# Kernel optimization log

Hardware: AMD Instinct MI355X
Metric: run time of the kernel (lower is better)

Reference implementation:

```python
import jax, jax.numpy as jnp
import numpy as np

E = 1024          # n_embed_dim
H = 64            # head_size = n_embed_dim // n_heads (16)

def setup_inputs() -> dict:
    key = jax.random.key(0)
    k_x, k_q, k_k, k_v = jax.random.split(key, 4)
    scale = 1.0 / np.sqrt(E)
    return {
        "x": jax.random.normal(k_x, (4, 2048, E), dtype=jnp.float32),
        "ln_gamma": jnp.ones((E,), jnp.float32),
        "ln_beta": jnp.zeros((E,), jnp.float32),
        # torch nn.Linear weights: [out_features, in_features]
        "Wq": jax.random.normal(k_q, (H, E), dtype=jnp.float32) * scale,
        "Wk": jax.random.normal(k_k, (H, E), dtype=jnp.float32) * scale,
        "Wv": jax.random.normal(k_v, (H, E), dtype=jnp.float32) * scale,
    }

def reference(x, ln_gamma, ln_beta, Wq, Wk, Wv):
    # LayerNorm over last dim (eps matches torch default 1e-5)
    mu = jnp.mean(x, axis=-1, keepdims=True)
    var = jnp.mean(jnp.square(x - mu), axis=-1, keepdims=True)
    xn = (x - mu) * jax.lax.rsqrt(var + 1e-5) * ln_gamma + ln_beta

    q = jnp.einsum('bse,he->bsh', xn, Wq)   # [B,S,H]
    k = jnp.einsum('bse,he->bsh', xn, Wk)
    v = jnp.einsum('bse,he->bsh', xn, Wv)

    scores = jnp.einsum('bqh,bkh->bqk', q, k) / jnp.sqrt(jnp.float32(H))
    S = x.shape[1]
    causal = jnp.tril(jnp.ones((S, S), dtype=bool))
    scores = jnp.where(causal, scores, -jnp.inf)
    attn = jax.nn.softmax(scores, axis=-1)
    return jnp.einsum('bqk,bkh->bqh', attn, v)
```

## Files before the change

### kernel.cpp

```cpp
#include <hip/hip_runtime.h>

#define E 1024
#define HH 64
#define BB 4
#define SS 2048
#define BS (BB*SS)
#define NSLOT 144

typedef unsigned short u16;
typedef short bf16x8 __attribute__((ext_vector_type(8)));
typedef float f32x4 __attribute__((ext_vector_type(4)));

#define LOG2E_O8 0.18033688011112042f

__device__ inline u16 f2bf(float f) {
    unsigned int u = __float_as_uint(f);
    unsigned int r = (u + 0x7FFFu + ((u >> 16) & 1u)) >> 16;
    return (u16)r;
}
__device__ inline float bf2f(u16 h) {
    return __uint_as_float(((unsigned int)h) << 16);
}

__global__ __launch_bounds__(256) void ln_wcast(const float* __restrict__ x,
        const float* __restrict__ gamma, const float* __restrict__ beta,
        const float* __restrict__ Wq, const float* __restrict__ Wk,
        const float* __restrict__ Wv,
        u16* __restrict__ xn, u16* __restrict__ wc) {
    const int t = threadIdx.x;
    if (blockIdx.x < 2048) {
        const int w = t >> 6, lane = t & 63;
        const size_t row = (size_t)blockIdx.x * 4 + w;
        const float4* xr = (const float4*)(x + row * E);
        float4 v[4];
        #pragma unroll
        for (int i = 0; i < 4; ++i) v[i] = xr[lane + 64 * i];
        float s = 0.f, sq = 0.f;
        #pragma unroll
        for (int i = 0; i < 4; ++i) {
            s  += v[i].x + v[i].y + v[i].z + v[i].w;
            sq += v[i].x*v[i].x + v[i].y*v[i].y + v[i].z*v[i].z + v[i].w*v[i].w;
        }
        #pragma unroll
        for (int off = 32; off > 0; off >>= 1) {
            s  += __shfl_xor(s,  off);
            sq += __shfl_xor(sq, off);
        }
        const float mean = s * (1.0f / E);
        const float var  = sq * (1.0f / E) - mean * mean;
        const float rstd = rsqrtf(var + 1e-5f);
        const float4* gr = (const float4*)gamma;
        const float4* br = (const float4*)beta;
        #pragma unroll
        for (int i = 0; i < 4; ++i) {
            const float4 g  = gr[lane + 64 * i];
            const float4 bt = br[lane + 64 * i];
            ushort4 o;
            o.x = f2bf((v[i].x - mean) * rstd * g.x + bt.x);
            o.y = f2bf((v[i].y - mean) * rstd * g.y + bt.y);
            o.z = f2bf((v[i].z - mean) * rstd * g.z + bt.z);
            o.w = f2bf((v[i].w - mean) * rstd * g.w + bt.w);
            *(ushort4*)(xn + row * E + (lane + 64 * i) * 4) = o;
        }
    } else {
        const int row = blockIdx.x - 2048;
        const float* src = (row < 64)  ? (Wq + (size_t)row * E)
                         : (row < 128) ? (Wk + (size_t)(row - 64) * E)
                                       : (Wv + (size_t)(row - 128) * E);
        const float sc = (row < 64) ? LOG2E_O8 : 1.0f;
        const float4 v = *(const float4*)(src + t * 4);
        ushort4 o;
        o.x = f2bf(v.x * sc); o.y = f2bf(v.y * sc);
        o.z = f2bf(v.z * sc); o.w = f2bf(v.w * sc);
        *(ushort4*)(wc + (size_t)row * E + t * 4) = o;
    }
}

__global__ __launch_bounds__(256) void qkv_mfma(const u16* __restrict__ xn,
        const u16* __restrict__ wc,
        u16* __restrict__ qb, u16* __restrict__ kb, u16* __restrict__ vt) {
    const int mb   = blockIdx.x >> 1;
    const int half = blockIdx.x & 1;
    const int row0 = mb * 32;
    const int t = threadIdx.x;
    const int w = t >> 6, lane = t & 63;
    const int quad = lane >> 4, r15 = lane & 15;
    const int mt = w >> 1, cgrp = w & 1;
    __shared__ u16 Xs[32 * 128];
    __shared__ u16 Ws[96 * 128];
    f32x4 acc[3] = {};
    const int xrow = mt * 16 + r15;

    for (int kc8 = 0; kc8 < 8; ++kc8) {
        __syncthreads();
        {
            const int row = t >> 3, ch = t & 7;
            #pragma unroll
            for (int hf = 0; hf < 2; ++hf) {
                const uint4 d = *(const uint4*)(xn + (size_t)(row0 + row) * E
                                                + kc8 * 128 + hf * 64 + ch * 8);
                *(uint4*)&Xs[row * 128 + hf * 64 + (ch ^ (row & 7)) * 8] = d;
            }
        }
        #pragma unroll
        for (int i = 0; i < 6; ++i) {
            const int idx = i * 256 + t;
            const int wl = idx >> 4, ch16 = idx & 15;
            const int hf = ch16 >> 3, ch = ch16 & 7;
            const uint4 d = *(const uint4*)(wc + (size_t)(half * 96 + wl) * E
                                            + kc8 * 128 + hf * 64 + ch * 8);
            *(uint4*)&Ws[wl * 128 + hf * 64 + (ch ^ (wl & 7)) * 8] = d;
        }
        __syncthreads();
        #pragma unroll
        for (int kk = 0; kk < 4; ++kk) {
            const int hf = kk >> 1, q4 = (kk & 1) * 4 + quad;
            const bf16x8 af = *(const bf16x8*)&Xs[xrow * 128 + hf * 64 + (q4 ^ (xrow & 7)) * 8];
            #pragma unroll
            for (int j = 0; j < 3; ++j) {
                const int wl = (cgrp * 3 + j) * 16 + r15;
                const bf16x8 bfr = *(const bf16x8*)&Ws[wl * 128 + hf * 64 + (q4 ^ (wl & 7)) * 8];
                acc[j] = __builtin_amdgcn_mfma_f32_16x16x32_bf16(af, bfr, acc[j], 0, 0, 0);
            }
        }
    }
    const int b    = row0 >> 11;
    const int key0 = row0 & 2047;
    #pragma unroll
    for (int j = 0; j < 3; ++j) {
        const int cg  = half * 96 + cgrp * 48 + j * 16 + r15;
        const int sel = cg >> 6;
        const int col = cg & 63;
        if (sel < 2) {
            u16* base = (sel == 0) ? qb : kb;
            #pragma unroll
            for (int r = 0; r < 4; ++r) {
                const size_t row = (size_t)row0 + mt * 16 + quad * 4 + r;
                base[row * HH + col] = f2bf(acc[j][r]);
            }
        } else {
            ushort4 pk;
            pk.x = f2bf(acc[j][0]); pk.y = f2bf(acc[j][1]);
            pk.z = f2bf(acc[j][2]); pk.w = f2bf(acc[j][3]);
            *(ushort4*)(vt + (size_t)b * HH * SS + (size_t)col * SS
                           + key0 + mt * 16 + quad * 4) = pk;
        }
    }
}

__global__ __launch_bounds__(256) void attn_partial(const u16* __restrict__ qb,
        const u16* __restrict__ kb, const u16* __restrict__ vt,
        u16* __restrict__ po, float* __restrict__ pl,
        float* __restrict__ out) {
    const int bid = blockIdx.x;
    const int b   = bid / NSLOT;
    const int s   = bid - b * NSLOT;
    int a = (int)((sqrtf(2.0f * s + 1.0f) - 1.0f) * 0.5f);
    while (2 * (a + 1) * (a + 2) <= s) ++a;
    while (2 * a * (a + 1) > s) --a;
    const int rem = s - 2 * a * (a + 1);
    const int r_  = rem / (a + 1);
    const int c   = rem - r_ * (a + 1);
    const int qt  = 4 * a + r_;
    const int nc   = a + 1;
    const int slot = b * NSLOT + s;
    const int q0   = qt << 6;
    const int t = threadIdx.x;
    const int w = t >> 6, lane = t & 63;
    const int quad = lane >> 4, r15 = lane & 15;

    __shared__ u16 Ks[4 * 64 * 64];
    __shared__ u16 VT[4 * 64 * 64];
    __shared__ u16 Ps[64 * 64];

    const size_t qrow = ((size_t)b * SS + q0 + w * 16 + r15) * HH;
    const bf16x8 qf0 = *(const bf16x8*)(qb + qrow + quad * 8);
    const bf16x8 qf1 = *(const bf16x8*)(qb + qrow + 32 + quad * 8);

    const int ntiles = min(c * 4 + 4, qt + 1) - c * 4;

    {
        const int row = t >> 2, ch0 = (t & 3) * 2;
        for (int tl = 0; tl < ntiles; ++tl) {
            const int kt = (c * 4 + tl) << 6;
            const uint4* srcK = (const uint4*)(kb + ((size_t)b * SS + kt + row) * HH + ch0 * 8);
            const uint4 k0 = srcK[0], k1 = srcK[1];
            *(uint4*)&Ks[tl * 4096 + row * 64 + ((ch0    ) ^ (row & 7)) * 8] = k0;
            *(uint4*)&Ks[tl * 4096 + row * 64 + ((ch0 + 1) ^ (row & 7)) * 8] = k1;
            const uint4* srcV = (const uint4*)(vt + (size_t)b * HH * SS + (size_t)row * SS
                                               + kt + ch0 * 8);
            const uint4 v0 = srcV[0], v1 = srcV[1];
            *(uint4*)&VT[tl * 4096 + row * 64 + ((ch0    ) ^ (row & 7)) * 8] = v0;
            *(uint4*)&VT[tl * 4096 + row * 64 + ((ch0 + 1) ^ (row & 7)) * 8] = v1;
        }
    }
    __syncthreads();

    f32x4 o[4] = {};
    float l_[4] = {0.f, 0.f, 0.f, 0.f};

    for (int tl = 0; tl < ntiles; ++tl) {
        const int tile = c * 4 + tl;
        const u16* KsT = &Ks[tl * 4096];
        const u16* VTT = &VT[tl * 4096];

        f32x4 s4[4] = {};
        #pragma unroll
        for (int nt = 0; nt < 4; ++nt) {
            const int krow = nt * 16 + r15;
            const bf16x8 k0 = *(const bf16x8*)&KsT[krow * 64 + ((    quad) ^ (krow & 7)) * 8];
            const bf16x8 k1 = *(const bf16x8*)&KsT[krow * 64 + ((4 + quad) ^ (krow & 7)) * 8];
            s4[nt] = __builtin_amdgcn_mfma_f32_16x16x32_bf16(qf0, k0, s4[nt], 0, 0, 0);
            s4[nt] = __builtin_amdgcn_mfma_f32_16x16x32_bf16(qf1, k1, s4[nt], 0, 0, 0);
        }
        if (tile == qt) {
            #pragma unroll
            for (int nt = 0; nt < 4; ++nt)
                #pragma unroll
                for (int r = 0; r < 4; ++r)
                    if (nt * 16 + r15 > w * 16 + quad * 4 + r) s4[nt][r] = -INFINITY;
        }

        float p[4][4];
        #pragma unroll
        for (int r = 0; r < 4; ++r) {
            #pragma unroll
            for (int nt = 0; nt < 4; ++nt)
                p[nt][r] = __builtin_amdgcn_exp2f(s4[nt][r]);
            l_[r] += (p[0][r] + p[1][r]) + (p[2][r] + p[3][r]);
        }

        #pragma unroll
        for (int nt = 0; nt < 4; ++nt)
            #pragma unroll
            for (int r = 0; r < 4; ++r) {
                const int prow = w * 16 + quad * 4 + r;
                const int col  = nt * 16 + r15;
                Ps[prow * 64 + (((col >> 3) ^ (prow & 7)) * 8) + (col & 7)] = f2bf(p[nt][r]);
            }
        const int arow = w * 16 + r15;
        const bf16x8 pf0 = *(const bf16x8*)&Ps[arow * 64 + ((    quad) ^ (arow & 7)) * 8];
        const bf16x8 pf1 = *(const bf16x8*)&Ps[arow * 64 + ((4 + quad) ^ (arow & 7)) * 8];

        #pragma unroll
        for (int ht = 0; ht < 4; ++ht) {
            const int vrow = ht * 16 + r15;
            const bf16x8 v0 = *(const bf16x8*)&VTT[vrow * 64 + ((    quad) ^ (vrow & 7)) * 8];
            const bf16x8 v1 = *(const bf16x8*)&VTT[vrow * 64 + ((4 + quad) ^ (vrow & 7)) * 8];
            o[ht] = __builtin_amdgcn_mfma_f32_16x16x32_bf16(pf0, v0, o[ht], 0, 0, 0);
            o[ht] = __builtin_amdgcn_mfma_f32_16x16x32_bf16(pf1, v1, o[ht], 0, 0, 0);
        }
    }

    #pragma unroll
    for (int r = 0; r < 4; ++r) {
        l_[r] += __shfl_xor(l_[r], 1); l_[r] += __shfl_xor(l_[r], 2);
        l_[r] += __shfl_xor(l_[r], 4); l_[r] += __shfl_xor(l_[r], 8);
    }

    if (nc == 1) {
        #pragma unroll
        for (int r = 0; r < 4; ++r) {
            const float inv = 1.0f / l_[r];
            const size_t orow = ((size_t)b * SS + q0 + w * 16 + quad * 4 + r) * HH;
            #pragma unroll
            for (int ht = 0; ht < 4; ++ht)
                out[orow + ht * 16 + r15] = o[ht][r] * inv;
        }
        return;
    }
    #pragma unroll
    for (int r = 0; r < 4; ++r) {
        const int q = w * 16 + quad * 4 + r;
        #pragma unroll
        for (int ht = 0; ht < 4; ++ht)
            po[(size_t)slot * 4096 + q * 64 + ht * 16 + r15] = f2bf(o[ht][r]);
        if (r15 == 0) pl[slot * 64 + q] = l_[r];
    }
}

__global__ __launch_bounds__(256) void attn_reduce(const u16* __restrict__ po,
        const float* __restrict__ pl, float* __restrict__ out) {
    const int bid = blockIdx.x;
    const int b = bid / 112, rem = bid - b * 112;
    const int qt = 4 + (rem >> 2), qq = rem & 3;
    const int a = qt >> 2, r_ = qt & 3;
    const int nc = a + 1;
    const int sbase = b * NSLOT + 2 * a * (a + 1) + r_ * (a + 1);
    const int t = threadIdx.x;
    const int h = t & 63, qr = t >> 6;
    #pragma unroll
    for (int i = 0; i < 4; ++i) {
        const int q = qq * 16 + qr * 4 + i;
        float osum = 0.f, lsum = 0.f;
        for (int cidx = 0; cidx < nc; ++cidx) {
            osum += bf2f(po[(size_t)(sbase + cidx) * 4096 + q * 64 + h]);
            lsum += pl[(sbase + cidx) * 64 + q];
        }
        out[((size_t)b * SS + (qt << 6) + q) * HH + h] = osum / lsum;
    }
}

extern "C" void kernel_launch(void* const* d_in, const int* in_sizes, int n_in,
                              void* d_out, int out_size, void* d_ws, size_t ws_size,
                              hipStream_t stream) {
    const float* x     = (const float*)d_in[0];
    const float* gamma = (const float*)d_in[1];
    const float* beta  = (const float*)d_in[2];
    const float* Wq    = (const float*)d_in[3];
    const float* Wk    = (const float*)d_in[4];
    const float* Wv    = (const float*)d_in[5];
    float* out = (float*)d_out;

    char* p = (char*)d_ws;
    u16*   xn   = (u16*)p;                         p += (size_t)BS * E * 2;
    u16*   wc   = (u16*)p;                         p += 393216;
    u16*   qb   = (u16*)p;                         p += (size_t)BS * HH * 2;
    u16*   kb   = (u16*)p;                         p += (size_t)BS * HH * 2;
    u16*   vt   = (u16*)p;                         p += (size_t)BS * HH * 2;
    u16*   po   = (u16*)p;                         p += (size_t)BB * NSLOT * 4096 * 2;
    float* pl   = (float*)p;

    ln_wcast    <<<2048 + 192,  256, 0, stream>>>(x, gamma, beta, Wq, Wk, Wv, xn, wc);
    qkv_mfma    <<<BS / 16,     256, 0, stream>>>(xn, wc, qb, kb, vt);
    attn_partial<<<BB * NSLOT,  256, 0, stream>>>(qb, kb, vt, po, pl, out);
    attn_reduce <<<BB * 112,    256, 0, stream>>>(po, pl, out);
}
```

Before: 118.8 us.

## Process two query tiles per attention block to reuse staged K/V tiles

Each attention_partial block now handles two adjacent query tiles against the same key chunk, so each K/V tile staged in LDS is used twice and the grid is halved. K and V fragments are hoisted out of the query loop into registers. In exchange, per-thread register use and work per block roughly double, and there are fewer blocks to spread across the CUs. Tiles above the diagonal are skipped for the lower query tile.

```diff
diff --git a/kernel.cpp b/kernel.cpp
--- a/kernel.cpp
+++ b/kernel.cpp
@@ -153,18 +153,16 @@
         u16* __restrict__ po, float* __restrict__ pl,
         float* __restrict__ out) {
     const int bid = blockIdx.x;
-    const int b   = bid / NSLOT;
-    const int s   = bid - b * NSLOT;
-    int a = (int)((sqrtf(2.0f * s + 1.0f) - 1.0f) * 0.5f);
-    while (2 * (a + 1) * (a + 2) <= s) ++a;
-    while (2 * a * (a + 1) > s) --a;
-    const int rem = s - 2 * a * (a + 1);
-    const int r_  = rem / (a + 1);
-    const int c   = rem - r_ * (a + 1);
-    const int qt  = 4 * a + r_;
-    const int nc   = a + 1;
-    const int slot = b * NSLOT + s;
-    const int q0   = qt << 6;
+    const int b   = bid / 72;
+    const int s2  = bid - b * 72;
+    int a = (int)((sqrtf(4.0f * s2 + 1.0f) - 1.0f) * 0.5f);
+    while ((a + 1) * (a + 2) <= s2) ++a;
+    while (a * (a + 1) > s2) --a;
+    const int rem = s2 - a * (a + 1);
+    const int rp  = rem / (a + 1);
+    const int c   = rem - rp * (a + 1);
+    const int qt0 = 4 * a + 2 * rp;
+    const int nc  = a + 1;
     const int t = threadIdx.x;
     const int w = t >> 6, lane = t & 63;
     const int quad = lane >> 4, r15 = lane & 15;
@@ -173,15 +171,19 @@
     __shared__ u16 VT[4 * 64 * 64];
     __shared__ u16 Ps[64 * 64];
 
-    const size_t qrow = ((size_t)b * SS + q0 + w * 16 + r15) * HH;
-    const bf16x8 qf0 = *(const bf16x8*)(qb + qrow + quad * 8);
-    const bf16x8 qf1 = *(const bf16x8*)(qb + qrow + 32 + quad * 8);
-
-    const int ntiles = min(c * 4 + 4, qt + 1) - c * 4;
+    bf16x8 qf0[2], qf1[2];
+    #pragma unroll
+    for (int qi = 0; qi < 2; ++qi) {
+        const size_t qrow = ((size_t)b * SS + (qt0 + qi) * 64 + w * 16 + r15) * HH;
+        qf0[qi] = *(const bf16x8*)(qb + qrow + quad * 8);
+        qf1[qi] = *(const bf16x8*)(qb + qrow + 32 + quad * 8);
+    }
+
+    const int ntmax = (c < a) ? 4 : (2 * rp + 2);
 
     {
         const int row = t >> 2, ch0 = (t & 3) * 2;
-        for (int tl = 0; tl < ntiles; ++tl) {
+        for (int tl = 0; tl < ntmax; ++tl) {
             const int kt = (c * 4 + tl) << 6;
             const uint4* srcK = (const uint4*)(kb + ((size_t)b * SS + kt + row) * HH + ch0 * 8);
             const uint4 k0 = srcK[0], k1 = srcK[1];
@@ -196,86 +198,103 @@
     }
     __syncthreads();
 
-    f32x4 o[4] = {};
-    float l_[4] = {0.f, 0.f, 0.f, 0.f};
-
-    for (int tl = 0; tl < ntiles; ++tl) {
+    f32x4 o[2][4] = {};
+    float l_[2][4] = {};
+
+    for (int tl = 0; tl < ntmax; ++tl) {
         const int tile = c * 4 + tl;
         const u16* KsT = &Ks[tl * 4096];
         const u16* VTT = &VT[tl * 4096];
 
-        f32x4 s4[4] = {};
+        bf16x8 kf0[4], kf1[4], vf0[4], vf1[4];
         #pragma unroll
         for (int nt = 0; nt < 4; ++nt) {
             const int krow = nt * 16 + r15;
-            const bf16x8 k0 = *(const bf16x8*)&KsT[krow * 64 + ((    quad) ^ (krow & 7)) * 8];
-            const bf16x8 k1 = *(const bf16x8*)&KsT[krow * 64 + ((4 + quad) ^ (krow & 7)) * 8];
-            s4[nt] = __builtin_amdgcn_mfma_f32_16x16x32_bf16(qf0, k0, s4[nt], 0, 0, 0);
-            s4[nt] = __builtin_amdgcn_mfma_f32_16x16x32_bf16(qf1, k1, s4[nt], 0, 0, 0);
-        }
-        if (tile == qt) {
+            kf0[nt] = *(const bf16x8*)&KsT[krow * 64 + ((    quad) ^ (krow & 7)) * 8];
+            kf1[nt] = *(const bf16x8*)&KsT[krow * 64 + ((4 + quad) ^ (krow & 7)) * 8];
+            vf0[nt] = *(const bf16x8*)&VTT[krow * 64 + ((    quad) ^ (krow & 7)) * 8];
+            vf1[nt] = *(const bf16x8*)&VTT[krow * 64 + ((4 + quad) ^ (krow & 7)) * 8];
+        }
+
+        #pragma unroll
+        for (int qi = 0; qi < 2; ++qi) {
+            const int qt_i = qt0 + qi;
+            if (tile > qt_i) continue;
+
+            f32x4 s4[4] = {};
+            #pragma unroll
+            for (int nt = 0; nt < 4; ++nt) {
+                s4[nt] = __builtin_amdgcn_mfma_f32_16x16x32_bf16(qf0[qi], kf0[nt], s4[nt], 0, 0, 0);
+                s4[nt] = __builtin_amdgcn_mfma_f32_16x16x32_bf16(qf1[qi], kf1[nt], s4[nt], 0, 0, 0);
+            }
+            if (tile == qt_i) {
+                #pragma unroll
+                for (int nt = 0; nt < 4; ++nt)
+                    #pragma unroll
+                    for (int r = 0; r < 4; ++r)
+                        if (nt * 16 + r15 > w * 16 + quad * 4 + r) s4[nt][r] = -INFINITY;
+            }
+
+            float p[4][4];
+            #pragma unroll
+            for (int r = 0; r < 4; ++r) {
+                #pragma unroll
+                for (int nt = 0; nt < 4; ++nt)
+                    p[nt][r] = __builtin_amdgcn_exp2f(s4[nt][r]);
+                l_[qi][r] += (p[0][r] + p[1][r]) + (p[2][r] + p[3][r]);
+            }
+
             #pragma unroll
             for (int nt = 0; nt < 4; ++nt)
                 #pragma unroll
-                for (int r = 0; r < 4; ++r)
-                    if (nt * 16 + r15 > w * 16 + quad * 4 + r) s4[nt][r] = -INFINITY;
-        }
-
-        float p[4][4];
+                for (int r = 0; r < 4; ++r) {
+                    const int prow = w * 16 + quad * 4 + r;
+                    const int col  = nt * 16 + r15;
+                    Ps[prow * 64 + (((col >> 3) ^ (prow & 7)) * 8) + (col & 7)] = f2bf(p[nt][r]);
+                }
+            const int arow = w * 16 + r15;
+            const bf16x8 pf0 = *(const bf16x8*)&Ps[arow * 64 + ((    quad) ^ (arow & 7)) * 8];
+            const bf16x8 pf1 = *(const bf16x8*)&Ps[arow * 64 + ((4 + quad) ^ (arow & 7)) * 8];
+
+            #pragma unroll
+            for (int ht = 0; ht < 4; ++ht) {
+                o[qi][ht] = __builtin_amdgcn_mfma_f32_16x16x32_bf16(pf0, vf0[ht], o[qi][ht], 0, 0, 0);
+                o[qi][ht] = __builtin_amdgcn_mfma_f32_16x16x32_bf16(pf1, vf1[ht], o[qi][ht], 0, 0, 0);
+            }
+        }
+    }
+
+    #pragma unroll
+    for (int qi = 0; qi < 2; ++qi)
         #pragma unroll
         for (int r = 0; r < 4; ++r) {
-            #pragma unroll
-            for (int nt = 0; nt < 4; ++nt)
-                p[nt][r] = __builtin_amdgcn_exp2f(s4[nt][r]);
-            l_[r] += (p[0][r] + p[1][r]) + (p[2][r] + p[3][r]);
-        }
-
-        #pragma unroll
-        for (int nt = 0; nt < 4; ++nt)
+            l_[qi][r] += __shfl_xor(l_[qi][r], 1); l_[qi][r] += __shfl_xor(l_[qi][r], 2);
+            l_[qi][r] += __shfl_xor(l_[qi][r], 4); l_[qi][r] += __shfl_xor(l_[qi][r], 8);
+        }
+
+    #pragma unroll
+    for (int qi = 0; qi < 2; ++qi) {
+        const int qt_i = qt0 + qi;
+        if (nc == 1) {
             #pragma unroll
             for (int r = 0; r < 4; ++r) {
-                const int prow = w * 16 + quad * 4 + r;
-                const int col  = nt * 16 + r15;
-                Ps[prow * 64 + (((col >> 3) ^ (prow & 7)) * 8) + (col & 7)] = f2bf(p[nt][r]);
-            }
-        const int arow = w * 16 + r15;
-        const bf16x8 pf0 = *(const bf16x8*)&Ps[arow * 64 + ((    quad) ^ (arow & 7)) * 8];
-        const bf16x8 pf1 = *(const bf16x8*)&Ps[arow * 64 + ((4 + quad) ^ (arow & 7)) * 8];
-
-        #pragma unroll
-        for (int ht = 0; ht < 4; ++ht) {
-            const int vrow = ht * 16 + r15;
-            const bf16x8 v0 = *(const bf16x8*)&VTT[vrow * 64 + ((    quad) ^ (vrow & 7)) * 8];
-            const bf16x8 v1 = *(const bf16x8*)&VTT[vrow * 64 + ((4 + quad) ^ (vrow & 7)) * 8];
-            o[ht] = __builtin_amdgcn_mfma_f32_16x16x32_bf16(pf0, v0, o[ht], 0, 0, 0);
-            o[ht] = __builtin_amdgcn_mfma_f32_16x16x32_bf16(pf1, v1, o[ht], 0, 0, 0);
-        }
-    }
-
-    #pragma unroll
-    for (int r = 0; r < 4; ++r) {
-        l_[r] += __shfl_xor(l_[r], 1); l_[r] += __shfl_xor(l_[r], 2);
-        l_[r] += __shfl_xor(l_[r], 4); l_[r] += __shfl_xor(l_[r], 8);
-    }
-
-    if (nc == 1) {
-        #pragma unroll
-        for (int r = 0; r < 4; ++r) {
-            const float inv = 1.0f / l_[r];
-            const size_t orow = ((size_t)b * SS + q0 + w * 16 + quad * 4 + r) * HH;
-            #pragma unroll
-            for (int ht = 0; ht < 4; ++ht)
-                out[orow + ht * 16 + r15] = o[ht][r] * inv;
-        }
-        return;
-    }
-    #pragma unroll
-    for (int r = 0; r < 4; ++r) {
-        const int q = w * 16 + quad * 4 + r;
-        #pragma unroll
-        for (int ht = 0; ht < 4; ++ht)
-            po[(size_t)slot * 4096 + q * 64 + ht * 16 + r15] = f2bf(o[ht][r]);
-        if (r15 == 0) pl[slot * 64 + q] = l_[r];
+                const float inv = 1.0f / l_[qi][r];
+                const size_t orow = ((size_t)b * SS + qt_i * 64 + w * 16 + quad * 4 + r) * HH;
+                #pragma unroll
+                for (int ht = 0; ht < 4; ++ht)
+                    out[orow + ht * 16 + r15] = o[qi][ht][r] * inv;
+            }
+        } else {
+            const int slot = b * NSLOT + 2 * a * (a + 1) + (2 * rp + qi) * (a + 1) + c;
+            #pragma unroll
+            for (int r = 0; r < 4; ++r) {
+                const int q = w * 16 + quad * 4 + r;
+                #pragma unroll
+                for (int ht = 0; ht < 4; ++ht)
+                    po[(size_t)slot * 4096 + q * 64 + ht * 16 + r15] = f2bf(o[qi][ht][r]);
+                if (r15 == 0) pl[slot * 64 + q] = l_[qi][r];
+            }
+        }
     }
 }
 
@@ -323,6 +342,6 @@
 
     ln_wcast    <<<2048 + 192,  256, 0, stream>>>(x, gamma, beta, Wq, Wk, Wv, xn, wc);
     qkv_mfma    <<<BS / 16,     256, 0, stream>>>(xn, wc, qb, kb, vt);
-    attn_partial<<<BB * NSLOT,  256, 0, stream>>>(qb, kb, vt, po, pl, out);
+    attn_partial<<<BB * 72,     256, 0, stream>>>(qb, kb, vt, po, pl, out);
     attn_reduce <<<BB * 112,    256, 0, stream>>>(po, pl, out);
 }
```

After: 118.2 us. About the same (-0.5%).
